# Kernel optimization log

Measured on AMD Instinct MI355X. Metric: run time of the kernel, lower is better.

## Reference

```python
import jax, jax.numpy as jnp
import numpy as np

BN_EPS = 1e-5


def _poly_ste(x):
    # Piecewise polynomial surrogate used for the activation STE backward:
    #   x < -1        -> -1
    #   x >= 1        -> 1
    out = jnp.where(x < -1, -1.0, x * x + 2.0 * x)
    out = jnp.where(x < 0, out, -x * x + 2.0 * x)
    out = jnp.where(x < 1, out, 1.0)
    return out


def setup_inputs() -> dict:
    key = jax.random.key(0)
    ks = jax.random.split(key, 7)
    N, C, H, W = 32, 128, 56, 56
    P = 128  # planes
    return {
        "x": jax.random.normal(ks[0], (N, C, H, W), dtype=jnp.float32),
        "weight": jax.random.normal(ks[1], (P, C, 3, 3), dtype=jnp.float32) * 0.05,
        "bias": jax.random.normal(ks[2], (P,), dtype=jnp.float32) * 0.05,
        "gamma": jax.random.uniform(ks[3], (P,), dtype=jnp.float32, minval=0.5, maxval=1.5),
        "beta": jax.random.normal(ks[4], (P,), dtype=jnp.float32) * 0.05,
        "running_mean": jax.random.normal(ks[5], (P,), dtype=jnp.float32) * 0.1,
        "running_var": jax.random.uniform(ks[6], (P,), dtype=jnp.float32, minval=0.5, maxval=1.5),
    }


def reference(x, weight, bias, gamma, beta, running_mean, running_var):
    # BinaryActivation: forward = sign(x), backward = d(poly)/dx (STE via detach trick)
    poly = _poly_ste(x)
    a = poly + jax.lax.stop_gradient(jnp.sign(x) - poly)

    # HardBinaryConv: weights binarized with straight-through sign; input already +/-1.
    wb = weight + jax.lax.stop_gradient(jnp.sign(weight) - weight)

    # 3x3 conv, stride 1, padding 1, NCHW / OIHW layout
    out = jax.lax.conv_general_dilated(
        a, wb,
        window_strides=(1, 1),
        padding=((1, 1), (1, 1)),
        dimension_numbers=("NCHW", "OIHW", "NCHW"),
    )
    out = out + bias[None, :, None, None]

    # BatchNorm2d in eval mode (running statistics)
    inv = gamma / jnp.sqrt(running_var + BN_EPS)
    out = out * inv[None, :, None, None] + (beta - running_mean * inv)[None, :, None, None]

    # Residual add (downsample=None, stride=1, inplanes==planes)
    return out + x
```

## Files before the change

kernel.cpp:

```cpp
#include <hip/hip_runtime.h>
#include <stdint.h>

#define N_  32
#define C_  128
#define H_  56
#define W_  56
#define HW_ 3136
#define P_  128
#define NPIX (N_*HW_)

using i32x4 = __attribute__((ext_vector_type(4))) int;

#define ABITS_BYTES (NPIX*16)
#define WI8_BYTES   (P_*1152)

__global__ __launch_bounds__(256) void pack_x_kernel(const float* __restrict__ x,
                                                     uint32_t* __restrict__ abits_w) {
    int b      = blockIdx.x;
    int j      = b & 3;
    int pairId = (b >> 2) * 256 + threadIdx.x;
    int n      = pairId / (HW_ / 2);
    int r      = (pairId % (HW_ / 2)) * 2;
    const float* px = x + ((size_t)n * C_ + j * 32) * HW_ + r;
    uint32_t w0 = 0, w1 = 0;
    #pragma unroll
    for (int c = 0; c < 32; ++c) {
        float2 v = *(const float2*)(px + (size_t)c * HW_);
        if (v.x >= 0.f) w0 |= 1u << c;
        if (v.y >= 0.f) w1 |= 1u << c;
    }
    int pix = n * HW_ + r;
    abits_w[(size_t)pix * 4 + j]       = w0;
    abits_w[(size_t)(pix + 1) * 4 + j] = w1;
}

__global__ __launch_bounds__(256) void wpack_kernel(const float* __restrict__ weight,
        const float* __restrict__ bias, const float* __restrict__ gamma,
        const float* __restrict__ beta, const float* __restrict__ mean,
        const float* __restrict__ var,
        uint32_t* __restrict__ wI8, float* __restrict__ invG, float* __restrict__ b0G) {
    int gid = blockIdx.x * 256 + threadIdx.x;
    int p   = gid / 288;
    int rem = gid % 288;
    int k   = rem * 4;
    int tp  = k >> 7;
    int c   = k & 127;
    uint32_t d = 0;
    #pragma unroll
    for (int i2 = 0; i2 < 4; ++i2) {
        float v = weight[((size_t)p * C_ + c + i2) * 9 + tp];
        uint32_t by = (v >= 0.f) ? 0x01u : 0xFFu;
        d |= by << (8 * i2);
    }
    wI8[gid] = d;
    if (blockIdx.x == 0 && threadIdx.x < P_) {
        int pp = threadIdx.x;
        float inv = gamma[pp] * rsqrtf(var[pp] + 1e-5f);
        invG[pp] = inv;
        b0G[pp]  = bias[pp] * inv + beta[pp] - mean[pp] * inv;
    }
}

__global__ __launch_bounds__(256) void bconv_kernel(
        const uint4* __restrict__ abits, const uint4* __restrict__ wI8v,
        const float* __restrict__ invG, const float* __restrict__ b0G,
        const float* __restrict__ x, float* __restrict__ out) {
    __shared__ uint4 actT[4 * 68 * 8];
    __shared__ uint4 sW[128 * 8];
    __shared__ float sInv[P_], sB0[P_];

    int tid = threadIdx.x;
    int img = blockIdx.x / 28;
    int rp  = blockIdx.x % 28;
    int r0  = rp * 2;

    if (tid < P_) { sInv[tid] = invG[tid]; sB0[tid] = b0G[tid]; }

    for (int cell = tid; cell < 4 * 68; cell += 256) {
        int rho  = cell & 3;
        int colL = cell >> 2;
        int h    = r0 - 1 + rho;
        int wv   = colL - 1;
        bool valid = ((unsigned)h < H_) && ((unsigned)wv < W_);
        uint4 bits = valid ? abits[img * HW_ + h * W_ + wv] : make_uint4(0u, 0u, 0u, 0u);
        uint32_t bwv[4] = {bits.x, bits.y, bits.z, bits.w};
        int base16 = (rho * 68 + colL) * 8;
        int sz = colL & 7;
        #pragma unroll
        for (int cb = 0; cb < 8; ++cb) {
            uint32_t hw16 = (bwv[cb >> 1] >> ((cb & 1) * 16)) & 0xFFFFu;
            uint4 dq;
            uint32_t n0 = hw16 & 0xF, n1 = (hw16 >> 4) & 0xF,
                     n2 = (hw16 >> 8) & 0xF, n3 = (hw16 >> 12) & 0xF;
            dq.x = 0xFFFFFFFFu ^ (((n0 * 0x204081u) & 0x01010101u) * 0xFEu);
            dq.y = 0xFFFFFFFFu ^ (((n1 * 0x204081u) & 0x01010101u) * 0xFEu);
            dq.z = 0xFFFFFFFFu ^ (((n2 * 0x204081u) & 0x01010101u) * 0xFEu);
            dq.w = 0xFFFFFFFFu ^ (((n3 * 0x204081u) & 0x01010101u) * 0xFEu);
            if (!valid) { dq.x = dq.y = dq.z = dq.w = 0u; }
            actT[base16 + (cb ^ sz)] = dq;
        }
    }

    int lane = tid & 63;
    int wi   = tid >> 6;
    int q    = lane >> 4;
    int l15  = lane & 15;
    int m0   = wi * 32;

    i32x4 acc[2][8];
    #pragma unroll
    for (int mi = 0; mi < 2; ++mi)
        #pragma unroll
        for (int j = 0; j < 8; ++j)
            #pragma unroll
            for (int e = 0; e < 4; ++e) acc[mi][j][e] = 0;

    int mA[2] = { m0 + l15, m0 + 16 + l15 };

    for (int t9 = 0; t9 < 9; ++t9) {
        __syncthreads();
        {
            int p = tid >> 1, half = tid & 1;
            const uint4* src = wI8v + (size_t)p * 72 + t9 * 8 + half * 4;
            #pragma unroll
            for (int g2 = 0; g2 < 4; ++g2)
                sW[p * 8 + ((half * 4 + g2) ^ (p & 7))] = src[g2];
        }
        __syncthreads();
        int dh = t9 / 3, dw = t9 % 3;
        #pragma unroll
        for (int ks = 0; ks < 2; ++ks) {
            i32x4 af[2];
            #pragma unroll
            for (int mi = 0; mi < 2; ++mi) {
                int m = mA[mi];
                af[mi] = *(const i32x4*)&sW[m * 8 + ((ks * 4 + q) ^ (m & 7))];
            }
            #pragma unroll
            for (int j = 0; j < 8; ++j) {
                int n    = j * 16 + l15;
                int colL = (n & 63) + dw;
                int rho  = (n >> 6) + dh;
                i32x4 bf = *(const i32x4*)&actT[(rho * 68 + colL) * 8 + ((ks * 4 + q) ^ (colL & 7))];
                acc[0][j] = __builtin_amdgcn_mfma_i32_16x16x64_i8(af[0], bf, acc[0][j], 0, 0, 0);
                acc[1][j] = __builtin_amdgcn_mfma_i32_16x16x64_i8(af[1], bf, acc[1][j], 0, 0, 0);
            }
        }
    }

    float invR[2][4], b0R[2][4];
    #pragma unroll
    for (int mi = 0; mi < 2; ++mi)
        #pragma unroll
        for (int reg = 0; reg < 4; ++reg) {
            int m = m0 + mi * 16 + q * 4 + reg;
            invR[mi][reg] = sInv[m];
            b0R[mi][reg]  = sB0[m];
        }
    #pragma unroll
    for (int j = 0; j < 8; ++j) {
        int n = j * 16 + l15;
        int w = n & 63;
        if (w < W_) {
            int orow = r0 + (n >> 6);
            size_t pixOff = (size_t)img * P_ * HW_ + (size_t)orow * W_ + w;
            #pragma unroll
            for (int mi = 0; mi < 2; ++mi)
                #pragma unroll
                for (int reg = 0; reg < 4; ++reg) {
                    int m = m0 + mi * 16 + q * 4 + reg;
                    size_t off = pixOff + (size_t)m * HW_;
                    out[off] = (float)acc[mi][j][reg] * invR[mi][reg] + b0R[mi][reg] + x[off];
                }
        }
    }
}

extern "C" void kernel_launch(void* const* d_in, const int* in_sizes, int n_in,
                              void* d_out, int out_size, void* d_ws, size_t ws_size,
                              hipStream_t stream) {
    const float* x      = (const float*)d_in[0];
    const float* weight = (const float*)d_in[1];
    const float* bias   = (const float*)d_in[2];
    const float* gamma  = (const float*)d_in[3];
    const float* beta   = (const float*)d_in[4];
    const float* mean   = (const float*)d_in[5];
    const float* var    = (const float*)d_in[6];
    float* out = (float*)d_out;

    uint8_t*  ws    = (uint8_t*)d_ws;
    uint32_t* abits = (uint32_t*)ws;
    uint32_t* wI8   = (uint32_t*)(ws + ABITS_BYTES);
    float*    invG  = (float*)(ws + ABITS_BYTES + WI8_BYTES);
    float*    b0G   = invG + P_;

    pack_x_kernel<<<(NPIX / 2) * 4 / 256, 256, 0, stream>>>(x, abits);
    wpack_kernel<<<144, 256, 0, stream>>>(weight, bias, gamma, beta, mean, var, wI8, invG, b0G);
    bconv_kernel<<<32 * 28, 256, 0, stream>>>((const uint4*)abits, (const uint4*)wI8,
                                              invG, b0G, x, out);
}
```

Baseline: 156.7 us.

## Load weight fragments directly from global into registers with double buffering

Removes the shared-memory weight staging and the two per-tap barriers. Each wave now loads its own weight MFMA operands straight from global memory into registers, prefetching the next tap while the current one computes. This cuts LDS traffic and synchronisation, at the cost of uncoalesced 16-byte global loads (served by L2) and extra registers.

Result: faster. 148.6 us (-5.2%).

```diff
diff --git a/kernel.cpp b/kernel.cpp
--- a/kernel.cpp
+++ b/kernel.cpp
@@ -66,7 +66,6 @@
         const float* __restrict__ invG, const float* __restrict__ b0G,
         const float* __restrict__ x, float* __restrict__ out) {
     __shared__ uint4 actT[4 * 68 * 8];
-    __shared__ uint4 sW[128 * 8];
     __shared__ float sInv[P_], sB0[P_];
 
     int tid = threadIdx.x;
@@ -107,6 +106,14 @@
     int l15  = lane & 15;
     int m0   = wi * 32;
 
+    i32x4 aw[2][2][2];
+    #pragma unroll
+    for (int mi = 0; mi < 2; ++mi)
+        #pragma unroll
+        for (int ks = 0; ks < 2; ++ks)
+            aw[0][mi][ks] = *(const i32x4*)&wI8v[(size_t)(m0 + mi*16 + l15) * 72
+                                                 + 0 * 8 + ks * 4 + q];
+
     i32x4 acc[2][8];
     #pragma unroll
     for (int mi = 0; mi < 2; ++mi)
@@ -115,35 +122,29 @@
             #pragma unroll
             for (int e = 0; e < 4; ++e) acc[mi][j][e] = 0;
 
-    int mA[2] = { m0 + l15, m0 + 16 + l15 };
+    __syncthreads();
 
     for (int t9 = 0; t9 < 9; ++t9) {
-        __syncthreads();
-        {
-            int p = tid >> 1, half = tid & 1;
-            const uint4* src = wI8v + (size_t)p * 72 + t9 * 8 + half * 4;
-            #pragma unroll
-            for (int g2 = 0; g2 < 4; ++g2)
-                sW[p * 8 + ((half * 4 + g2) ^ (p & 7))] = src[g2];
-        }
-        __syncthreads();
+        int nb = t9 & 1;
+        if (t9 < 8) {
+            #pragma unroll
+            for (int mi = 0; mi < 2; ++mi)
+                #pragma unroll
+                for (int ks = 0; ks < 2; ++ks)
+                    aw[nb ^ 1][mi][ks] = *(const i32x4*)&wI8v[(size_t)(m0 + mi*16 + l15) * 72
+                                                              + (t9 + 1) * 8 + ks * 4 + q];
+        }
         int dh = t9 / 3, dw = t9 % 3;
         #pragma unroll
         for (int ks = 0; ks < 2; ++ks) {
-            i32x4 af[2];
-            #pragma unroll
-            for (int mi = 0; mi < 2; ++mi) {
-                int m = mA[mi];
-                af[mi] = *(const i32x4*)&sW[m * 8 + ((ks * 4 + q) ^ (m & 7))];
-            }
             #pragma unroll
             for (int j = 0; j < 8; ++j) {
                 int n    = j * 16 + l15;
                 int colL = (n & 63) + dw;
                 int rho  = (n >> 6) + dh;
                 i32x4 bf = *(const i32x4*)&actT[(rho * 68 + colL) * 8 + ((ks * 4 + q) ^ (colL & 7))];
-                acc[0][j] = __builtin_amdgcn_mfma_i32_16x16x64_i8(af[0], bf, acc[0][j], 0, 0, 0);
-                acc[1][j] = __builtin_amdgcn_mfma_i32_16x16x64_i8(af[1], bf, acc[1][j], 0, 0, 0);
+                acc[0][j] = __builtin_amdgcn_mfma_i32_16x16x64_i8(aw[nb][0][ks], bf, acc[0][j], 0, 0, 0);
+                acc[1][j] = __builtin_amdgcn_mfma_i32_16x16x64_i8(aw[nb][1][ks], bf, acc[1][j], 0, 0, 0);
             }
         }
     }
```
